# Optimization experiments

Hardware: AMD Instinct MI355X
Metric: run time of the kernel (lower is better)

Reference implementation:

```python
import jax, jax.numpy as jnp
import numpy as np

N = 32768       # nodes
E = 65536       # directed edges
B = 512         # graphs (N // B = 64 atoms each)
DIM = 64
NUM_FEAT = 14
EDGE_DIM = 4
NET_HID = 128
CONV_STEPS = 12
S2S_STEPS = 3
NSTEM = 1024
NUM_OUT_STEM = 105

leaky = lambda v: jax.nn.leaky_relu(v, 0.01)


def setup_inputs():
    key = jax.random.key(0)
    ks = jax.random.split(key, 30)
    p = lambda i, shape, s=0.1: jax.random.normal(ks[i], shape, jnp.float32) * s
    return {
        'x': jax.random.normal(ks[0], (N, NUM_FEAT), jnp.float32),
        'edge_attr': jax.random.uniform(ks[1], (E, EDGE_DIM), jnp.float32),
        'edge_index': jax.random.randint(ks[2], (2, E), 0, N),
        'batch': jnp.arange(N, dtype=jnp.int32) // (N // B),  # sorted graph ids, all graphs non-empty
        'stem_idx': jax.random.randint(ks[3], (NSTEM,), 0, N),
        'lin0_w': p(4, (DIM, NUM_FEAT)), 'lin0_b': p(5, (DIM,)),
        'net_w1': p(6, (NET_HID, EDGE_DIM)), 'net_b1': p(7, (NET_HID,)),
        'net_w2': p(8, (DIM * DIM, NET_HID), 0.05), 'net_b2': p(9, (DIM * DIM,), 0.05),
        'conv_root': p(10, (DIM, DIM)), 'conv_bias': p(11, (DIM,)),
        'gru_w_ih': p(12, (3 * DIM, DIM)), 'gru_w_hh': p(13, (3 * DIM, DIM)),
        'gru_b_ih': p(14, (3 * DIM,)), 'gru_b_hh': p(15, (3 * DIM,)),
        'lin1_w': p(16, (8 * DIM, DIM)), 'lin1_b': p(17, (8 * DIM,)),
        'lin2_w': p(18, (NUM_OUT_STEM, 8 * DIM)), 'lin2_b': p(19, (NUM_OUT_STEM,)),
        's2s_w_ih': p(20, (4 * DIM, 2 * DIM)), 's2s_w_hh': p(21, (4 * DIM, DIM)),
        's2s_b_ih': p(22, (4 * DIM,)), 's2s_b_hh': p(23, (4 * DIM,)),
        'lin3_w': p(24, (1, 2 * DIM)), 'lin3_b': p(25, (1,)),
    }


def reference(x, edge_attr, edge_index, batch, stem_idx,
              lin0_w, lin0_b, net_w1, net_b1, net_w2, net_b2,
              conv_root, conv_bias, gru_w_ih, gru_w_hh, gru_b_ih, gru_b_hh,
              lin1_w, lin1_b, lin2_w, lin2_b,
              s2s_w_ih, s2s_w_hh, s2s_b_ih, s2s_b_hh, lin3_w, lin3_b):
    src, dst = edge_index[0], edge_index[1]

    out = leaky(x @ lin0_w.T + lin0_b)               # [N, DIM]
    h = out

    # edge-conditioned weights: constant across conv steps (edge_attr fixed), hoist
    W = (leaky(edge_attr @ net_w1.T + net_b1) @ net_w2.T + net_b2).reshape(E, DIM, DIM)

    deg = jax.ops.segment_sum(jnp.ones((E,), jnp.float32), dst, num_segments=N)
    inv_deg = (1.0 / jnp.maximum(deg, 1.0))[:, None]

    def step(carry, _):
        out, h = carry
        # NNConv: gather src feats, per-edge matmul, scatter-mean to dst, plus root term
        msg = jnp.einsum('ei,eio->eo', out[src], W)                           # [E, DIM]
        agg = jax.ops.segment_sum(msg, dst, num_segments=N) * inv_deg        # scatter-mean
        m = leaky(agg + out @ conv_root + conv_bias)
        # GRU cell (torch gate order r, z, n)
        gi = m @ gru_w_ih.T + gru_b_ih
        gh = h @ gru_w_hh.T + gru_b_hh
        ir, iz, i_n = jnp.split(gi, 3, axis=-1)
        hr, hz, hn = jnp.split(gh, 3, axis=-1)
        r = jax.nn.sigmoid(ir + hr)
        z = jax.nn.sigmoid(iz + hz)
        n = jnp.tanh(i_n + r * hn)
        h_new = (1.0 - z) * n + z * h
        return (h_new, h_new), None

    (out, h), _ = jax.lax.scan(step, (out, h), None, length=CONV_STEPS)

    # per-stem head (stem_idx = precomputed flat node indices)
    stem_feat = out[stem_idx]                                                # [NSTEM, DIM]
    per_stem_out = leaky(stem_feat @ lin1_w.T + lin1_b) @ lin2_w.T + lin2_b  # [NSTEM, 105]

    # Set2Set readout (LSTM with torch gate order i, f, g, o)
    q_star = jnp.zeros((B, 2 * DIM), jnp.float32)
    hh = jnp.zeros((B, DIM), jnp.float32)
    cc = jnp.zeros((B, DIM), jnp.float32)
    for _ in range(S2S_STEPS):
        gates = q_star @ s2s_w_ih.T + s2s_b_ih + hh @ s2s_w_hh.T + s2s_b_hh
        gi_, gf_, gg_, go_ = jnp.split(gates, 4, axis=-1)
        cc = jax.nn.sigmoid(gf_) * cc + jax.nn.sigmoid(gi_) * jnp.tanh(gg_)
        hh = jax.nn.sigmoid(go_) * jnp.tanh(cc)
        q = hh                                                               # [B, DIM]
        e = jnp.sum(out * q[batch], axis=-1)                                 # [N]
        emax = jax.ops.segment_max(e, batch, num_segments=B)
        ee = jnp.exp(e - emax[batch])
        a = ee / jax.ops.segment_sum(ee, batch, num_segments=B)[batch]       # segment softmax
        r_read = jax.ops.segment_sum(a[:, None] * out, batch, num_segments=B)
        q_star = jnp.concatenate([q, r_read], axis=-1)

    sout = q_star @ lin3_w.T + lin3_b                                        # [B, 1]
    return sout, per_stem_out


if __name__ == '__main__':
    o = reference(**setup_inputs())
    print(o[0].shape, o[1].shape)
```

## Files before the change

kernel.cpp:

```cpp
#include <hip/hip_runtime.h>
#include <hip/hip_bf16.h>

#define N_NODES   32768
#define N_EDGES   65536
#define NGRAPH    512
#define DIM       64
#define NFEAT     14
#define NHID      128
#define WCOLS     4096
#define NSTEM     1024
#define NOUT      105

typedef __attribute__((ext_vector_type(8))) short short8;
typedef __attribute__((ext_vector_type(4))) float f32x4;

__device__ __forceinline__ float bf2f(unsigned int u16) {
  union { unsigned int i; float f; } c; c.i = u16 << 16; return c.f;
}
__device__ __forceinline__ unsigned short f2bf(float f) {
  union { float f; unsigned int i; } c; c.f = f;
  return (unsigned short)((c.i + 0x7fffu + ((c.i >> 16) & 1u)) >> 16);
}
__device__ __forceinline__ float leaky(float x) { return x > 0.f ? x : 0.01f * x; }
__device__ __forceinline__ float sigm(float x) { return 1.f / (1.f + expf(-x)); }

constexpr size_t ALN(size_t x) { return (x + 255) & ~(size_t)255; }

constexpr size_t OFF_HIDP = 0;
constexpr size_t SZ_HIDP  = (size_t)N_EDGES * NHID * 2;
constexpr size_t OFF_T2T  = ALN(OFF_HIDP + SZ_HIDP);
constexpr size_t SZ_T2T   = (size_t)WCOLS * NHID * 2;
constexpr size_t OFF_B2T  = ALN(OFF_T2T + SZ_T2T);
constexpr size_t SZ_B2T   = (size_t)WCOLS * 4;
constexpr size_t OFF_STATE= ALN(OFF_B2T + SZ_B2T);
constexpr size_t SZ_STATE = (size_t)N_NODES * DIM * 4;
constexpr size_t OFF_AGG  = ALN(OFF_STATE + SZ_STATE);
constexpr size_t SZ_AGG   = SZ_STATE;
constexpr size_t OFF_IDEG = ALN(OFF_AGG + SZ_AGG);
constexpr size_t SZ_IDEG  = (size_t)N_NODES * 4;
constexpr size_t OFF_CNT  = ALN(OFF_IDEG + SZ_IDEG);
constexpr size_t SZ_CNT   = (size_t)N_NODES * 4;
constexpr size_t OFF_RP   = ALN(OFF_CNT + SZ_CNT);
constexpr size_t SZ_RP    = (size_t)(N_NODES + 1) * 4;
constexpr size_t OFF_CUR  = ALN(OFF_RP + SZ_RP);
constexpr size_t SZ_CUR   = (size_t)N_NODES * 4;
constexpr size_t OFF_SRCP = ALN(OFF_CUR + SZ_CUR);
constexpr size_t SZ_SRCP  = (size_t)N_EDGES * 4;
constexpr size_t OFF_DSTP = ALN(OFF_SRCP + SZ_SRCP);
constexpr size_t SZ_DSTP  = (size_t)N_EDGES * 4;
constexpr size_t OFF_EPOS = ALN(OFF_DSTP + SZ_DSTP);
constexpr size_t SZ_EPOS  = (size_t)N_EDGES * 4;
constexpr size_t OFF_BW1  = ALN(OFF_EPOS + SZ_EPOS);
constexpr size_t SZ_BW1   = 256 * 64 * 2;
constexpr size_t OFF_BW2  = ALN(OFF_BW1 + SZ_BW1);
constexpr size_t SZ_BW2   = 192 * 64 * 2;
constexpr size_t OFF_WIH  = ALN(OFF_BW2 + SZ_BW2);
constexpr size_t SZ_WIH   = 128 * 256 * 4;
constexpr size_t OFF_WHH  = ALN(OFF_WIH + SZ_WIH);
constexpr size_t SZ_WHH   = 64 * 256 * 4;
constexpr size_t OFF_S8   = ALN(OFF_WHH + SZ_WHH);
constexpr size_t SZ_S8    = (size_t)N_NODES * 64;
constexpr size_t OFF_SSC  = ALN(OFF_S8 + SZ_S8);
constexpr size_t SZ_SSC   = (size_t)N_NODES * 4;
constexpr size_t OFF_SCL  = ALN(OFF_SSC + SZ_SSC);
constexpr size_t SZ_SCL   = (size_t)N_EDGES * 64 * 4;
constexpr size_t OFF_WT   = ALN(OFF_SCL + SZ_SCL);

__global__ void k_deg(const int* __restrict__ dst, int* __restrict__ cnt) {
  int e = blockIdx.x * 256 + threadIdx.x;
  atomicAdd(&cnt[dst[e]], 1);
}
__global__ __launch_bounds__(1024) void k_scan(const int* __restrict__ cnt,
                                               int* __restrict__ rp,
                                               int* __restrict__ cur,
                                               float* __restrict__ ideg) {
  __shared__ int part[1024];
  const int t = threadIdx.x, base = t * 32;
  int s = 0;
  for (int i = 0; i < 32; ++i) s += cnt[base + i];
  part[t] = s;
  __syncthreads();
  for (int off = 1; off < 1024; off <<= 1) {
    int v = (t >= off) ? part[t - off] : 0;
    __syncthreads();
    part[t] += v;
    __syncthreads();
  }
  int run = part[t] - s;
  for (int i = 0; i < 32; ++i) {
    int c = cnt[base + i];
    rp[base + i] = run; cur[base + i] = run;
    ideg[base + i] = 1.0f / fmaxf((float)c, 1.0f);
    run += c;
  }
  if (t == 1023) rp[N_NODES] = run;
}
__global__ void k_permute(const int* __restrict__ src, const int* __restrict__ dst,
                          int* __restrict__ cur, int* __restrict__ src_p,
                          int* __restrict__ dst_p, int* __restrict__ epos) {
  int e = blockIdx.x * 256 + threadIdx.x;
  int d = dst[e];
  int p = atomicAdd(&cur[d], 1);
  src_p[p] = src[e]; dst_p[p] = d; epos[e] = p;
}
__global__ void k_prep_t2(const float* __restrict__ w2, const float* __restrict__ b2,
                          unsigned short* __restrict__ T2t, float* __restrict__ b2t) {
  int gid = blockIdx.x * 256 + threadIdx.x;
  int r = gid >> 7, h = gid & 127;
  int srow = (r & 63) * 64 + (r >> 6);
  T2t[gid] = f2bf(w2[(size_t)srow * 128 + h]);
  if (h == 0) b2t[r] = b2[srow];
}
__global__ void k_prep_gru(const float* __restrict__ root, const float* __restrict__ whh,
                           const float* __restrict__ wih,
                           unsigned short* __restrict__ BW1, unsigned short* __restrict__ BW2) {
  int gid = blockIdx.x * 256 + threadIdx.x;
  if (gid >= 64 * 448) return;
  int i = gid / 448, c = gid % 448;
  if (c < 64)        BW1[c * 64 + i] = f2bf(root[i * 64 + c]);
  else if (c < 256)  BW1[c * 64 + i] = f2bf(whh[(c - 64) * 64 + i]);
  else               BW2[(c - 256) * 64 + i] = f2bf(wih[(c - 256) * 64 + i]);
}
__global__ void k_prep_s2s(const float* __restrict__ wih, const float* __restrict__ whh,
                           float* __restrict__ wihT, float* __restrict__ whhT) {
  int gid = blockIdx.x * 256 + threadIdx.x;
  if (gid < 32768) { int j = gid >> 8, k = gid & 255; wihT[gid] = wih[k * 128 + j]; }
  else { int g2 = gid - 32768; int j = g2 >> 8, k = g2 & 255; whhT[g2] = whh[k * 64 + j]; }
}
__global__ void k_lin0(const float* __restrict__ x, const float* __restrict__ w,
                       const float* __restrict__ b, float* __restrict__ state) {
  int gid = blockIdx.x * 256 + threadIdx.x;
  int n = gid >> 6, o = gid & 63;
  float acc = b[o];
  #pragma unroll
  for (int f = 0; f < NFEAT; ++f) acc += x[(size_t)n * NFEAT + f] * w[o * NFEAT + f];
  state[gid] = leaky(acc);
}
__global__ void k_hidden(const float* __restrict__ ea, const float* __restrict__ w1,
                         const float* __restrict__ b1, const int* __restrict__ epos,
                         unsigned short* __restrict__ hid_p) {
  int gid = blockIdx.x * 256 + threadIdx.x;
  int e = gid >> 7, h = gid & 127;
  float acc = b1[h];
  #pragma unroll
  for (int d = 0; d < 4; ++d) acc += ea[(size_t)e * 4 + d] * w1[h * 4 + d];
  hid_p[(size_t)epos[e] * 128 + h] = f2bf(leaky(acc));
}
__global__ __launch_bounds__(256) void k_qstate(const float* __restrict__ state,
                                                char* __restrict__ s8,
                                                float* __restrict__ sscale) {
  __shared__ char q8[4][64];
  __shared__ float scs[4];
  const int t = threadIdx.x, wv = t >> 6, ln = t & 63;
  const int n = blockIdx.x * 4 + wv;
  float v = state[(size_t)n * 64 + ln];
  float m = fabsf(v);
  #pragma unroll
  for (int off = 1; off < 64; off <<= 1) m = fmaxf(m, __shfl_xor(m, off));
  float inv = m > 0.f ? 127.f / m : 0.f;
  q8[wv][ln] = (char)(int)rintf(v * inv);
  if (ln == 0) scs[wv] = m * (1.f / 127.f);
  __syncthreads();
  if (t < 64) {
    int w2 = t >> 4, c = t & 15;
    reinterpret_cast<int*>(s8)[((size_t)(blockIdx.x * 4 + w2)) * 16 + c] =
        reinterpret_cast<const int*>(q8[w2])[c];
  }
  if (t < 4) sscale[blockIdx.x * 4 + t] = scs[t];
}

#define WG_PAD 136
__global__ __launch_bounds__(256) void k_wgemm(const unsigned short* __restrict__ A,
                                               const unsigned short* __restrict__ Bt,
                                               const float* __restrict__ b2t,
                                               unsigned char* __restrict__ W8,
                                               float* __restrict__ SCL) {
  __shared__ __align__(16) unsigned short As[64 * WG_PAD];
  __shared__ __align__(16) unsigned short Bs[64 * WG_PAD];
  __shared__ __align__(16) char pk[64][64];
  const int nb = blockIdx.x, mb = blockIdx.y, t = threadIdx.x;
  #pragma unroll
  for (int j = 0; j < 4; ++j) {
    int c = t + 256 * j;
    int row = c >> 4, col8 = (c & 15) * 8;
    *reinterpret_cast<uint4*>(&As[row * WG_PAD + col8]) =
        *reinterpret_cast<const uint4*>(A + (size_t)(mb * 64 + row) * 128 + col8);
    *reinterpret_cast<uint4*>(&Bs[row * WG_PAD + col8]) =
        *reinterpret_cast<const uint4*>(Bt + (size_t)(nb * 64 + row) * 128 + col8);
  }
  __syncthreads();
  const int wv = t >> 6, ln = t & 63, r = ln & 15, g = ln >> 4;
  f32x4 acc[4] = {};
  #pragma unroll
  for (int ks = 0; ks < 4; ++ks) {
    int kk = ks * 32 + g * 8;
    short8 a = *reinterpret_cast<const short8*>(&As[(wv * 16 + r) * WG_PAD + kk]);
    #pragma unroll
    for (int nt = 0; nt < 4; ++nt) {
      short8 b = *reinterpret_cast<const short8*>(&Bs[(nt * 16 + r) * WG_PAD + kk]);
      acc[nt] = __builtin_amdgcn_mfma_f32_16x16x32_bf16(a, b, acc[nt], 0, 0, 0);
    }
  }
  float bias[4];
  #pragma unroll
  for (int nt = 0; nt < 4; ++nt) bias[nt] = b2t[nb * 64 + nt * 16 + r];
  #pragma unroll
  for (int j = 0; j < 4; ++j) {
    int e_l = wv * 16 + g * 4 + j;
    float w[4], m = 0.f;
    #pragma unroll
    for (int nt = 0; nt < 4; ++nt) { w[nt] = acc[nt][j] + bias[nt]; m = fmaxf(m, fabsf(w[nt])); }
    m = fmaxf(m, __shfl_xor(m, 1)); m = fmaxf(m, __shfl_xor(m, 2));
    m = fmaxf(m, __shfl_xor(m, 4)); m = fmaxf(m, __shfl_xor(m, 8));
    float inv = m > 0.f ? 127.f / m : 0.f;
    #pragma unroll
    for (int nt = 0; nt < 4; ++nt)
      pk[e_l][nt * 16 + r] = (char)(int)rintf(w[nt] * inv);
    if (r == 0) {
      size_t e8 = (size_t)mb * 64 + e_l;
      SCL[e8 * 64 + nb] = m * (1.f / 127.f);
    }
  }
  __syncthreads();
  {
    int e_l = t >> 2, jc = t & 3;
    size_t e8 = (size_t)mb * 64 + e_l;
    *reinterpret_cast<uint4*>(W8 + e8 * 4096 + jc * 1024 + nb * 16) =
        *reinterpret_cast<const uint4*>(&pk[e_l][jc * 16]);
  }
}

__device__ __forceinline__ int dot64(const uint4* __restrict__ wp, const int* __restrict__ s) {
  int u = 0;
  #pragma unroll
  for (int j = 0; j < 4; ++j) {
    uint4 v = wp[j * 64];
    u = __builtin_amdgcn_sdot4((int)v.x, s[j * 4 + 0], u, false);
    u = __builtin_amdgcn_sdot4((int)v.y, s[j * 4 + 1], u, false);
    u = __builtin_amdgcn_sdot4((int)v.z, s[j * 4 + 2], u, false);
    u = __builtin_amdgcn_sdot4((int)v.w, s[j * 4 + 3], u, false);
  }
  return u;
}

__global__ __launch_bounds__(256) void k_msg_csr(const unsigned char* __restrict__ W8,
                                                 const float* __restrict__ SCL,
                                                 const char* __restrict__ s8,
                                                 const float* __restrict__ sscale,
                                                 int lim8,
                                                 const int* __restrict__ rp,
                                                 const int* __restrict__ src_p,
                                                 const float* __restrict__ ideg,
                                                 float* __restrict__ agg) {
  const int wv = threadIdx.x >> 6, ln = threadIdx.x & 63;
  const int d = blockIdx.x * 4 + wv;
  int k0 = rp[d], k1 = rp[d + 1];
  if (k1 > lim8) k1 = lim8;
  float acc = 0.f;
  int k = k0;
  for (; k + 2 <= k1; k += 2) {
    const uint4* wA = reinterpret_cast<const uint4*>(W8 + (size_t)k * 4096 + ln * 16);
    const uint4* wB = reinterpret_cast<const uint4*>(W8 + (size_t)(k + 1) * 4096 + ln * 16);
    int sA = __builtin_amdgcn_readfirstlane(src_p[k]);
    int sB = __builtin_amdgcn_readfirstlane(src_p[k + 1]);
    const int* rA = reinterpret_cast<const int*>(s8 + (size_t)sA * 64);
    const int* rB = reinterpret_cast<const int*>(s8 + (size_t)sB * 64);
    float fA = SCL[(size_t)k * 64 + ln] * sscale[sA];
    float fB = SCL[(size_t)k * 64 + 64 + ln] * sscale[sB];
    int uA = dot64(wA, rA);
    int uB = dot64(wB, rB);
    acc = fmaf((float)uA, fA, acc);
    acc = fmaf((float)uB, fB, acc);
  }
  if (k < k1) {
    const uint4* wA = reinterpret_cast<const uint4*>(W8 + (size_t)k * 4096 + ln * 16);
    int sA = __builtin_amdgcn_readfirstlane(src_p[k]);
    const int* rA = reinterpret_cast<const int*>(s8 + (size_t)sA * 64);
    float fA = SCL[(size_t)k * 64 + ln] * sscale[sA];
    acc = fmaf((float)dot64(wA, rA), fA, acc);
  }
  agg[(size_t)d * 64 + ln] = acc * ideg[d];
}

#define WM_PAD 136
__global__ __launch_bounds__(256) void k_wmsg(const unsigned short* __restrict__ hid,
                                              const unsigned short* __restrict__ T2t,
                                              const float* __restrict__ b2t,
                                              const float* __restrict__ state,
                                              const int* __restrict__ srcs,
                                              const int* __restrict__ dsts,
                                              const float* __restrict__ ideg,
                                              int e0,
                                              float* __restrict__ agg) {
  __shared__ __align__(16) unsigned short As[64 * WM_PAD];
  __shared__ __align__(16) unsigned short Bs[2][64 * WM_PAD];
  __shared__ __align__(16) float Ss[64][68];
  __shared__ int dstl[64]; __shared__ float idgl[64];
  __shared__ int srcl[64];
  const int t = threadIdx.x;
  const int eb = blockIdx.x * 64;
  if (t < 64) {
    int e = e0 + eb + t;
    srcl[t] = srcs[e];
    int d = dsts[e]; dstl[t] = d; idgl[t] = ideg[d];
  }
  __syncthreads();
  #pragma unroll
  for (int j = 0; j < 4; ++j) {
    int c = t + 256 * j;
    int row = c >> 4, col8 = (c & 15) * 8;
    *reinterpret_cast<uint4*>(&As[row * WM_PAD + col8]) =
        *reinterpret_cast<const uint4*>(hid + (size_t)(eb + row) * 128 + col8);
  }
  #pragma unroll
  for (int j = 0; j < 4; ++j) {
    int c = t + 256 * j;
    int row = c >> 4, q = (c & 15) * 4;
    *reinterpret_cast<float4*>(&Ss[row][q]) =
        *reinterpret_cast<const float4*>(state + (size_t)srcl[row] * 64 + q);
  }
  #pragma unroll
  for (int j = 0; j < 4; ++j) {
    int c = t + 256 * j;
    int row = c >> 4, col8 = (c & 15) * 8;
    *reinterpret_cast<uint4*>(&Bs[0][row * WM_PAD + col8]) =
        *reinterpret_cast<const uint4*>(T2t + (size_t)row * 128 + col8);
  }
  __syncthreads();
  const int wv = t >> 6, ln = t & 63, r = ln & 15, g = ln >> 4;
  for (int nb = 0; nb < 64; ++nb) {
    const int cur = nb & 1;
    if (nb + 1 < 64) {
      #pragma unroll
      for (int j = 0; j < 4; ++j) {
        int c = t + 256 * j;
        int row = c >> 4, col8 = (c & 15) * 8;
        *reinterpret_cast<uint4*>(&Bs[cur ^ 1][row * WM_PAD + col8]) =
            *reinterpret_cast<const uint4*>(T2t + (size_t)((nb + 1) * 64 + row) * 128 + col8);
      }
    }
    f32x4 acc[4] = {};
    #pragma unroll
    for (int ks = 0; ks < 4; ++ks) {
      int kk = ks * 32 + g * 8;
      short8 a = *reinterpret_cast<const short8*>(&As[(wv * 16 + r) * WM_PAD + kk]);
      #pragma unroll
      for (int nt = 0; nt < 4; ++nt) {
        short8 b = *reinterpret_cast<const short8*>(&Bs[cur][(nt * 16 + r) * WM_PAD + kk]);
        acc[nt] = __builtin_amdgcn_mfma_f32_16x16x32_bf16(a, b, acc[nt], 0, 0, 0);
      }
    }
    float bias[4];
    #pragma unroll
    for (int nt = 0; nt < 4; ++nt) bias[nt] = b2t[nb * 64 + nt * 16 + r];
    float pj[4];
    #pragma unroll
    for (int j = 0; j < 4; ++j) {
      int row = wv * 16 + g * 4 + j;
      float p = 0.f;
      #pragma unroll
      for (int nt = 0; nt < 4; ++nt)
        p += (acc[nt][j] + bias[nt]) * Ss[row][nt * 16 + r];
      pj[j] = p;
    }
    #pragma unroll
    for (int j = 0; j < 4; ++j) {
      float p = pj[j];
      p += __shfl_xor(p, 1); p += __shfl_xor(p, 2);
      p += __shfl_xor(p, 4); p += __shfl_xor(p, 8);
      pj[j] = p;
    }
    if (r == 0) {
      #pragma unroll
      for (int j = 0; j < 4; ++j) {
        int row = wv * 16 + g * 4 + j;
        atomicAdd(&agg[(size_t)dstl[row] * 64 + nb], pj[j] * idgl[row]);
      }
    }
    __syncthreads();
  }
}

#define KPAD 72
__global__ __launch_bounds__(512, 1) void k_gru(const float* __restrict__ agg,
                                                float* __restrict__ state,
                                                const unsigned short* __restrict__ BW1,
                                                const unsigned short* __restrict__ BW2,
                                                const float* __restrict__ conv_bias,
                                                const float* __restrict__ b_ih,
                                                const float* __restrict__ b_hh,
                                                char* __restrict__ s8,
                                                float* __restrict__ sscale) {
  __shared__ __align__(16) unsigned short As[128 * KPAD];
  __shared__ __align__(16) unsigned short Ms[128 * KPAD];
  __shared__ __align__(16) unsigned short B1s[256 * KPAD];
  __shared__ __align__(16) unsigned short B2s[192 * KPAD];
  const int t = threadIdx.x;
  const int rowbase = blockIdx.x * 128;
  #pragma unroll
  for (int j = 0; j < 2; ++j) {
    int c = t + 512 * j;
    int row = c >> 3, col8 = (c & 7) * 8;
    const float* sp = state + (size_t)(rowbase + row) * 64 + col8;
    float4 f0 = *reinterpret_cast<const float4*>(sp);
    float4 f1 = *reinterpret_cast<const float4*>(sp + 4);
    short8 hv;
    hv[0] = (short)f2bf(f0.x); hv[1] = (short)f2bf(f0.y);
    hv[2] = (short)f2bf(f0.z); hv[3] = (short)f2bf(f0.w);
    hv[4] = (short)f2bf(f1.x); hv[5] = (short)f2bf(f1.y);
    hv[6] = (short)f2bf(f1.z); hv[7] = (short)f2bf(f1.w);
    *reinterpret_cast<short8*>(&As[row * KPAD + col8]) = hv;
  }
  #pragma unroll
  for (int j = 0; j < 4; ++j) {
    int c = t + 512 * j;
    int row = c >> 3, col8 = (c & 7) * 8;
    *reinterpret_cast<uint4*>(&B1s[row * KPAD + col8]) =
        *reinterpret_cast<const uint4*>(BW1 + row * 64 + col8);
  }
  #pragma unroll
  for (int j = 0; j < 3; ++j) {
    int c = t + 512 * j;
    int row = c >> 3, col8 = (c & 7) * 8;
    *reinterpret_cast<uint4*>(&B2s[row * KPAD + col8]) =
        *reinterpret_cast<const uint4*>(BW2 + row * 64 + col8);
  }
  __syncthreads();
  const int wv = t >> 6, ln = t & 63, r = ln & 15, g = ln >> 4;
  f32x4 acc1[16] = {};
  #pragma unroll
  for (int ks = 0; ks < 2; ++ks) {
    int kk = ks * 32 + g * 8;
    short8 a = *reinterpret_cast<const short8*>(&As[(wv * 16 + r) * KPAD + kk]);
    #pragma unroll
    for (int nt = 0; nt < 16; ++nt) {
      short8 b = *reinterpret_cast<const short8*>(&B1s[(nt * 16 + r) * KPAD + kk]);
      acc1[nt] = __builtin_amdgcn_mfma_f32_16x16x32_bf16(a, b, acc1[nt], 0, 0, 0);
    }
  }
  #pragma unroll
  for (int nt = 0; nt < 4; ++nt) {
    int col = nt * 16 + r;
    float cb = conv_bias[col];
    #pragma unroll
    for (int j = 0; j < 4; ++j) {
      int lrow = wv * 16 + g * 4 + j;
      float mv = agg[(size_t)(rowbase + lrow) * 64 + col] + acc1[nt][j] + cb;
      Ms[lrow * KPAD + col] = f2bf(leaky(mv));
    }
  }
  __syncthreads();
  f32x4 acc2[12] = {};
  #pragma unroll
  for (int ks = 0; ks < 2; ++ks) {
    int kk = ks * 32 + g * 8;
    short8 a = *reinterpret_cast<const short8*>(&Ms[(wv * 16 + r) * KPAD + kk]);
    #pragma unroll
    for (int nt = 0; nt < 12; ++nt) {
      short8 b = *reinterpret_cast<const short8*>(&B2s[(nt * 16 + r) * KPAD + kk]);
      acc2[nt] = __builtin_amdgcn_mfma_f32_16x16x32_bf16(a, b, acc2[nt], 0, 0, 0);
    }
  }
  float hnew[4][4];
  #pragma unroll
  for (int nt = 0; nt < 4; ++nt) {
    int o = nt * 16 + r;
    float bir = b_ih[o],       bhr = b_hh[o];
    float biz = b_ih[64 + o],  bhz = b_hh[64 + o];
    float bin = b_ih[128 + o], bhn = b_hh[128 + o];
    #pragma unroll
    for (int j = 0; j < 4; ++j) {
      size_t gidx = (size_t)(rowbase + wv * 16 + g * 4 + j) * 64 + o;
      float rr = sigm(acc2[nt][j] + bir + acc1[4 + nt][j] + bhr);
      float zz = sigm(acc2[4 + nt][j] + biz + acc1[8 + nt][j] + bhz);
      float nn = tanhf(acc2[8 + nt][j] + bin + rr * (acc1[12 + nt][j] + bhn));
      float hold = state[gidx];
      float hv = (1.f - zz) * nn + zz * hold;
      state[gidx] = hv;
      hnew[nt][j] = hv;
    }
  }
  char* s8t = (char*)As;
  #pragma unroll
  for (int j = 0; j < 4; ++j) {
    float mx = 0.f;
    #pragma unroll
    for (int nt = 0; nt < 4; ++nt) mx = fmaxf(mx, fabsf(hnew[nt][j]));
    mx = fmaxf(mx, __shfl_xor(mx, 1)); mx = fmaxf(mx, __shfl_xor(mx, 2));
    mx = fmaxf(mx, __shfl_xor(mx, 4)); mx = fmaxf(mx, __shfl_xor(mx, 8));
    float inv = mx > 0.f ? 127.f / mx : 0.f;
    int lrow = wv * 16 + g * 4 + j;
    #pragma unroll
    for (int nt = 0; nt < 4; ++nt)
      s8t[lrow * 64 + nt * 16 + r] = (char)(int)rintf(hnew[nt][j] * inv);
    if (r == 0) sscale[rowbase + lrow] = mx * (1.f / 127.f);
  }
  __syncthreads();
  {
    int row = t >> 2, c = t & 3;
    *reinterpret_cast<uint4*>(s8 + ((size_t)(rowbase + row)) * 64 + c * 16) =
        *reinterpret_cast<const uint4*>(s8t + row * 64 + c * 16);
  }
}

__global__ __launch_bounds__(256) void k_s2s(const float* __restrict__ state,
                                             const float* __restrict__ wihT,
                                             const float* __restrict__ whhT,
                                             const float* __restrict__ b_ih,
                                             const float* __restrict__ b_hh,
                                             const float* __restrict__ lin3_w,
                                             const float* __restrict__ lin3_b,
                                             float* __restrict__ d_out) {
  __shared__ float tile[64 * 65];
  __shared__ float qs[128], hhs[64], ccs[64], gates[256], attw[64];
  const int g = blockIdx.x, t = threadIdx.x;
  for (int c = t; c < 64 * 64; c += 256) {
    int row = c >> 6, col = c & 63;
    tile[row * 65 + col] = state[(size_t)(g * 64 + row) * 64 + col];
  }
  if (t < 128) qs[t] = 0.f;
  if (t < 64) { hhs[t] = 0.f; ccs[t] = 0.f; }
  __syncthreads();
  for (int it = 0; it < 3; ++it) {
    float acc = b_ih[t] + b_hh[t];
    for (int j = 0; j < 128; ++j) acc += qs[j] * wihT[j * 256 + t];
    for (int j = 0; j < 64; ++j)  acc += hhs[j] * whhT[j * 256 + t];
    gates[t] = acc;
    __syncthreads();
    if (t < 64) {
      float ci = sigm(gates[t]), cf = sigm(gates[64 + t]);
      float cg = tanhf(gates[128 + t]), co = sigm(gates[192 + t]);
      float c2 = cf * ccs[t] + ci * cg;
      ccs[t] = c2;
      float h2 = co * tanhf(c2);
      hhs[t] = h2; qs[t] = h2;
    }
    __syncthreads();
    if (t < 64) {
      float e = 0.f;
      for (int o = 0; o < 64; ++o) e += tile[t * 65 + o] * qs[o];
      float m = e;
      for (int off = 32; off; off >>= 1) m = fmaxf(m, __shfl_xor(m, off));
// ... 40 lines not shown
      float4 x3 = *reinterpret_cast<const float4*>(wr + i + 12);
      a0 += x0.x*feat[i]    + x0.y*feat[i+1]  + x0.z*feat[i+2]  + x0.w*feat[i+3];
      a1 += x1.x*feat[i+4]  + x1.y*feat[i+5]  + x1.z*feat[i+6]  + x1.w*feat[i+7];
      a2 += x2.x*feat[i+8]  + x2.y*feat[i+9]  + x2.z*feat[i+10] + x2.w*feat[i+11];
      a3 += x3.x*feat[i+12] + x3.y*feat[i+13] + x3.z*feat[i+14] + x3.w*feat[i+15];
    }
    hidl[t] = leaky(a0 + a1 + a2 + a3 + b1[t]);
  }
  __syncthreads();
  if (t < 4 * NOUT) {
    int o = t >> 2, q = t & 3;
    const float* wr = w2 + (size_t)o * 512 + q * 128;
    const float* hr = hidl + q * 128;
    float a0 = 0.f, a1 = 0.f, a2 = 0.f, a3 = 0.f;
    #pragma unroll
    for (int kk = 0; kk < 128; kk += 16) {
      float4 x0 = *reinterpret_cast<const float4*>(wr + kk);
      float4 x1 = *reinterpret_cast<const float4*>(wr + kk + 4);
      float4 x2 = *reinterpret_cast<const float4*>(wr + kk + 8);
      float4 x3 = *reinterpret_cast<const float4*>(wr + kk + 12);
      a0 += x0.x*hr[kk]    + x0.y*hr[kk+1]  + x0.z*hr[kk+2]  + x0.w*hr[kk+3];
      a1 += x1.x*hr[kk+4]  + x1.y*hr[kk+5]  + x1.z*hr[kk+6]  + x1.w*hr[kk+7];
      a2 += x2.x*hr[kk+8]  + x2.y*hr[kk+9]  + x2.z*hr[kk+10] + x2.w*hr[kk+11];
      a3 += x3.x*hr[kk+12] + x3.y*hr[kk+13] + x3.z*hr[kk+14] + x3.w*hr[kk+15];
    }
    float p = a0 + a1 + a2 + a3;
    p += __shfl_xor(p, 1); p += __shfl_xor(p, 2);
    if (q == 0) d_out[512 + (size_t)s * NOUT + o] = p + b2[o];
  }
}

extern "C" void kernel_launch(void* const* d_in, const int* in_sizes, int n_in,
                              void* d_out, int out_size, void* d_ws, size_t ws_size,
                              hipStream_t stream) {
  (void)in_sizes; (void)n_in; (void)out_size;
  if (ws_size < OFF_WT) return;

  long pe8 = (long)((ws_size - OFF_WT) / 4096);
  if (pe8 > N_EDGES) pe8 = N_EDGES;
  pe8 &= ~63L;
  const int LIM8 = (int)pe8;
  const int TE = N_EDGES - LIM8;

  const float* x         = (const float*)d_in[0];
  const float* edge_attr = (const float*)d_in[1];
  const int*   eidx      = (const int*)d_in[2];
  const int*   stem_idx  = (const int*)d_in[4];
  const float* lin0_w = (const float*)d_in[5];
  const float* lin0_b = (const float*)d_in[6];
  const float* net_w1 = (const float*)d_in[7];
  const float* net_b1 = (const float*)d_in[8];
  const float* net_w2 = (const float*)d_in[9];
  const float* net_b2 = (const float*)d_in[10];
  const float* conv_root = (const float*)d_in[11];
  const float* conv_bias = (const float*)d_in[12];
  const float* gru_w_ih = (const float*)d_in[13];
  const float* gru_w_hh = (const float*)d_in[14];
  const float* gru_b_ih = (const float*)d_in[15];
  const float* gru_b_hh = (const float*)d_in[16];
  const float* lin1_w = (const float*)d_in[17];
  const float* lin1_b = (const float*)d_in[18];
  const float* lin2_w = (const float*)d_in[19];
  const float* lin2_b = (const float*)d_in[20];
  const float* s2s_w_ih = (const float*)d_in[21];
  const float* s2s_w_hh = (const float*)d_in[22];
  const float* s2s_b_ih = (const float*)d_in[23];
  const float* s2s_b_hh = (const float*)d_in[24];
  const float* lin3_w = (const float*)d_in[25];
  const float* lin3_b = (const float*)d_in[26];

  char* ws = (char*)d_ws;
  unsigned short* hid_p = (unsigned short*)(ws + OFF_HIDP);
  unsigned short* T2t  = (unsigned short*)(ws + OFF_T2T);
  float*          b2t  = (float*)(ws + OFF_B2T);
  float*          state= (float*)(ws + OFF_STATE);
  float*          agg  = (float*)(ws + OFF_AGG);
  float*          ideg = (float*)(ws + OFF_IDEG);
  int*            cnt  = (int*)(ws + OFF_CNT);
  int*            rp   = (int*)(ws + OFF_RP);
  int*            cur  = (int*)(ws + OFF_CUR);
  int*            src_p= (int*)(ws + OFF_SRCP);
  int*            dst_p= (int*)(ws + OFF_DSTP);
  int*            epos = (int*)(ws + OFF_EPOS);
  unsigned short* BW1  = (unsigned short*)(ws + OFF_BW1);
  unsigned short* BW2  = (unsigned short*)(ws + OFF_BW2);
  float*          wihT = (float*)(ws + OFF_WIH);
  float*          whhT = (float*)(ws + OFF_WHH);
  char*           s8   = (char*)(ws + OFF_S8);
  float*          sscale = (float*)(ws + OFF_SSC);
  float*          SCL  = (float*)(ws + OFF_SCL);
  unsigned char*  W8   = (unsigned char*)(ws + OFF_WT);
  float* out = (float*)d_out;

  const int* src = eidx;
  const int* dst = eidx + N_EDGES;

  hipMemsetAsync(cnt, 0, SZ_CNT, stream);
  k_deg<<<N_EDGES / 256, 256, 0, stream>>>(dst, cnt);
  k_scan<<<1, 1024, 0, stream>>>(cnt, rp, cur, ideg);
  k_permute<<<N_EDGES / 256, 256, 0, stream>>>(src, dst, cur, src_p, dst_p, epos);
  k_prep_t2<<<(WCOLS * NHID) / 256, 256, 0, stream>>>(net_w2, net_b2, T2t, b2t);
  k_prep_gru<<<112, 256, 0, stream>>>(conv_root, gru_w_hh, gru_w_ih, BW1, BW2);
  k_prep_s2s<<<192, 256, 0, stream>>>(s2s_w_ih, s2s_w_hh, wihT, whhT);
  k_lin0<<<(N_NODES * DIM) / 256, 256, 0, stream>>>(x, lin0_w, lin0_b, state);
  k_qstate<<<N_NODES / 4, 256, 0, stream>>>(state, s8, sscale);
  k_hidden<<<(N_EDGES * NHID) / 256, 256, 0, stream>>>(edge_attr, net_w1, net_b1,
                                                       epos, hid_p);
  if (LIM8 > 0)
    k_wgemm<<<dim3(WCOLS / 64, LIM8 / 64), 256, 0, stream>>>(hid_p, T2t, b2t, W8, SCL);

  for (int s = 0; s < 12; ++s) {
    k_msg_csr<<<N_NODES / 4, 256, 0, stream>>>(W8, SCL, s8, sscale, LIM8,
                                               rp, src_p, ideg, agg);
    if (TE > 0)
      k_wmsg<<<(TE + 63) / 64, 256, 0, stream>>>(hid_p + (size_t)LIM8 * NHID, T2t, b2t,
                                                 state, src_p, dst_p, ideg, LIM8, agg);
    k_gru<<<N_NODES / 128, 512, 0, stream>>>(agg, state, BW1, BW2, conv_bias,
                                             gru_b_ih, gru_b_hh, s8, sscale);
  }

  k_s2s<<<NGRAPH, 256, 0, stream>>>(state, wihT, whhT, s2s_b_ih, s2s_b_hh,
                                    lin3_w, lin3_b, out);
  k_stem<<<NSTEM, 512, 0, stream>>>(state, stem_idx, lin1_w, lin1_b,
                                    lin2_w, lin2_b, out);
}
```

Measured before the change: 1.981 ms.

## Switch message pass to edge-parallel chunks with output-major int8 weight layout

Replaces the per-destination CSR message kernel with an edge-parallel kernel in which each wave handles 16 consecutive sorted edges. The quantized weight tensor and its scales are re-laid out so that each lane reads a contiguous 64-byte row per edge, instead of strided 16-byte pieces. Destination segments that straddle chunk boundaries are merged with atomics, and interior segments are stored directly. Because accumulation now relies on atomics, agg is zeroed once up front and cleared inside the GRU kernel after it is read, replacing per-step overwrites. This is meant to fix load imbalance across nodes with uneven degree and to improve memory access patterns, at the cost of extra atomics and writes to agg.

```diff
diff --git a/kernel.cpp b/kernel.cpp
--- a/kernel.cpp
+++ b/kernel.cpp
@@ -216,25 +216,22 @@
     #pragma unroll
     for (int nt = 0; nt < 4; ++nt)
       pk[e_l][nt * 16 + r] = (char)(int)rintf(w[nt] * inv);
-    if (r == 0) {
-      size_t e8 = (size_t)mb * 64 + e_l;
-      SCL[e8 * 64 + nb] = m * (1.f / 127.f);
-    }
+    if (r == 0) SCL[(size_t)mb * 4096 + nb * 64 + e_l] = m * (1.f / 127.f);
   }
   __syncthreads();
   {
-    int e_l = t >> 2, jc = t & 3;
-    size_t e8 = (size_t)mb * 64 + e_l;
-    *reinterpret_cast<uint4*>(W8 + e8 * 4096 + jc * 1024 + nb * 16) =
-        *reinterpret_cast<const uint4*>(&pk[e_l][jc * 16]);
-  }
-}
-
-__device__ __forceinline__ int dot64(const uint4* __restrict__ wp, const int* __restrict__ s) {
+    int e_l = t >> 2, q4 = t & 3;
+    *reinterpret_cast<uint4*>(W8 + (size_t)mb * 262144 + (size_t)nb * 4096 +
+                              e_l * 64 + q4 * 16) =
+        *reinterpret_cast<const uint4*>(&pk[e_l][q4 * 16]);
+  }
+}
+
+__device__ __forceinline__ int dot64c(const uint4* __restrict__ wp, const int* __restrict__ s) {
   int u = 0;
   #pragma unroll
   for (int j = 0; j < 4; ++j) {
-    uint4 v = wp[j * 64];
+    uint4 v = wp[j];
     u = __builtin_amdgcn_sdot4((int)v.x, s[j * 4 + 0], u, false);
     u = __builtin_amdgcn_sdot4((int)v.y, s[j * 4 + 1], u, false);
     u = __builtin_amdgcn_sdot4((int)v.z, s[j * 4 + 2], u, false);
@@ -243,43 +240,42 @@
   return u;
 }
 
-__global__ __launch_bounds__(256) void k_msg_csr(const unsigned char* __restrict__ W8,
-                                                 const float* __restrict__ SCL,
-                                                 const char* __restrict__ s8,
-                                                 const float* __restrict__ sscale,
-                                                 int lim8,
-                                                 const int* __restrict__ rp,
-                                                 const int* __restrict__ src_p,
-                                                 const float* __restrict__ ideg,
-                                                 float* __restrict__ agg) {
+__global__ __launch_bounds__(256) void k_msg_edge(const unsigned char* __restrict__ W8,
+                                                  const float* __restrict__ SCL,
+                                                  const char* __restrict__ s8,
+                                                  const float* __restrict__ sscale,
+                                                  int lim8,
+                                                  const int* __restrict__ src_p,
+                                                  const int* __restrict__ dst_p,
+                                                  const float* __restrict__ ideg,
+                                                  float* __restrict__ agg) {
   const int wv = threadIdx.x >> 6, ln = threadIdx.x & 63;
-  const int d = blockIdx.x * 4 + wv;
-  int k0 = rp[d], k1 = rp[d + 1];
-  if (k1 > lim8) k1 = lim8;
+  const int kbase = (blockIdx.x * 4 + wv) * 16;
+  if (kbase >= lim8) return;
+  const int svv = src_p[kbase + (ln & 15)];
+  const int dvv = dst_p[kbase + (ln & 15)];
   float acc = 0.f;
-  int k = k0;
-  for (; k + 2 <= k1; k += 2) {
-    const uint4* wA = reinterpret_cast<const uint4*>(W8 + (size_t)k * 4096 + ln * 16);
-    const uint4* wB = reinterpret_cast<const uint4*>(W8 + (size_t)(k + 1) * 4096 + ln * 16);
-    int sA = __builtin_amdgcn_readfirstlane(src_p[k]);
-    int sB = __builtin_amdgcn_readfirstlane(src_p[k + 1]);
-    const int* rA = reinterpret_cast<const int*>(s8 + (size_t)sA * 64);
-    const int* rB = reinterpret_cast<const int*>(s8 + (size_t)sB * 64);
-    float fA = SCL[(size_t)k * 64 + ln] * sscale[sA];
-    float fB = SCL[(size_t)k * 64 + 64 + ln] * sscale[sB];
-    int uA = dot64(wA, rA);
-    int uB = dot64(wB, rB);
-    acc = fmaf((float)uA, fA, acc);
-    acc = fmaf((float)uB, fB, acc);
-  }
-  if (k < k1) {
-    const uint4* wA = reinterpret_cast<const uint4*>(W8 + (size_t)k * 4096 + ln * 16);
-    int sA = __builtin_amdgcn_readfirstlane(src_p[k]);
-    const int* rA = reinterpret_cast<const int*>(s8 + (size_t)sA * 64);
-    float fA = SCL[(size_t)k * 64 + ln] * sscale[sA];
-    acc = fmaf((float)dot64(wA, rA), fA, acc);
-  }
-  agg[(size_t)d * 64 + ln] = acc * ideg[d];
+  int dcur = __builtin_amdgcn_readfirstlane(__shfl(dvv, 0));
+  bool first = true;
+  #pragma unroll 4
+  for (int i = 0; i < 16; ++i) {
+    const int k = kbase + i;
+    const int eb = k >> 6, el = k & 63;
+    const uint4* wp = reinterpret_cast<const uint4*>(
+        W8 + (size_t)eb * 262144 + (size_t)ln * 4096 + el * 64);
+    const int s  = __builtin_amdgcn_readfirstlane(__shfl(svv, i));
+    const int dk = __builtin_amdgcn_readfirstlane(__shfl(dvv, i));
+    const int* rs = reinterpret_cast<const int*>(s8 + (size_t)s * 64);
+    const float f = SCL[(size_t)eb * 4096 + ln * 64 + el] * sscale[s];
+    if (dk != dcur) {
+      float outv = acc * ideg[dcur];
+      if (first) atomicAdd(&agg[(size_t)dcur * 64 + ln], outv);
+      else       agg[(size_t)dcur * 64 + ln] = outv;
+      first = false; acc = 0.f; dcur = dk;
+    }
+    acc = fmaf((float)dot64c(wp, rs), f, acc);
+  }
+  atomicAdd(&agg[(size_t)dcur * 64 + ln], acc * ideg[dcur]);
 }
 
 #define WM_PAD 136
@@ -382,7 +378,7 @@
 }
 
 #define KPAD 72
-__global__ __launch_bounds__(512, 1) void k_gru(const float* __restrict__ agg,
+__global__ __launch_bounds__(512, 1) void k_gru(float* __restrict__ agg,
                                                 float* __restrict__ state,
                                                 const unsigned short* __restrict__ BW1,
                                                 const unsigned short* __restrict__ BW2,
@@ -445,7 +441,9 @@
     #pragma unroll
     for (int j = 0; j < 4; ++j) {
       int lrow = wv * 16 + g * 4 + j;
-      float mv = agg[(size_t)(rowbase + lrow) * 64 + col] + acc1[nt][j] + cb;
+      size_t aidx = (size_t)(rowbase + lrow) * 64 + col;
+      float mv = agg[aidx] + acc1[nt][j] + cb;
+      agg[aidx] = 0.f;
       Ms[lrow * KPAD + col] = f2bf(leaky(mv));
     }
   }
@@ -678,6 +676,7 @@
   const int* dst = eidx + N_EDGES;
 
   hipMemsetAsync(cnt, 0, SZ_CNT, stream);
+  hipMemsetAsync(agg, 0, SZ_AGG, stream);
   k_deg<<<N_EDGES / 256, 256, 0, stream>>>(dst, cnt);
   k_scan<<<1, 1024, 0, stream>>>(cnt, rp, cur, ideg);
   k_permute<<<N_EDGES / 256, 256, 0, stream>>>(src, dst, cur, src_p, dst_p, epos);
@@ -692,8 +691,9 @@
     k_wgemm<<<dim3(WCOLS / 64, LIM8 / 64), 256, 0, stream>>>(hid_p, T2t, b2t, W8, SCL);
 
   for (int s = 0; s < 12; ++s) {
-    k_msg_csr<<<N_NODES / 4, 256, 0, stream>>>(W8, SCL, s8, sscale, LIM8,
-                                               rp, src_p, ideg, agg);
+    if (LIM8 > 0)
+      k_msg_edge<<<(LIM8 + 63) / 64, 256, 0, stream>>>(W8, SCL, s8, sscale, LIM8,
+                                                       src_p, dst_p, ideg, agg);
     if (TE > 0)
       k_wmsg<<<(TE + 63) / 64, 256, 0, stream>>>(hid_p + (size_t)LIM8 * NHID, T2t, b2t,
                                                  state, src_p, dst_p, ideg, LIM8, agg);
```

Measured after the change: 2.284 ms. 1.15x slower.

## Pre-swizzle GRU weights into MFMA fragment layout and read from global

Applied to the files above, without the earlier changes.

The GRU weight matrices are pre-packed into the per-lane MFMA B-fragment order, so each wave loads its B operands straight from global or L2 instead of staging them in LDS. Dropping that staging shrinks LDS per block, which allows smaller 64-row, 256-thread blocks and more blocks per CU. The k_wgemm launch is also split into two half-sized launches. The risk is repeated global reads of the weights by every block in place of shared LDS reuse.

```diff
diff --git a/kernel.cpp b/kernel.cpp
--- a/kernel.cpp
+++ b/kernel.cpp
@@ -51,9 +51,9 @@
 constexpr size_t OFF_EPOS = ALN(OFF_DSTP + SZ_DSTP);
 constexpr size_t SZ_EPOS  = (size_t)N_EDGES * 4;
 constexpr size_t OFF_BW1  = ALN(OFF_EPOS + SZ_EPOS);
-constexpr size_t SZ_BW1   = 256 * 64 * 2;
+constexpr size_t SZ_BW1   = 32 * 64 * 8 * 2;
 constexpr size_t OFF_BW2  = ALN(OFF_BW1 + SZ_BW1);
-constexpr size_t SZ_BW2   = 192 * 64 * 2;
+constexpr size_t SZ_BW2   = 24 * 64 * 8 * 2;
 constexpr size_t OFF_WIH  = ALN(OFF_BW2 + SZ_BW2);
 constexpr size_t SZ_WIH   = 128 * 256 * 4;
 constexpr size_t OFF_WHH  = ALN(OFF_WIH + SZ_WIH);
@@ -113,13 +113,22 @@
 }
 __global__ void k_prep_gru(const float* __restrict__ root, const float* __restrict__ whh,
                            const float* __restrict__ wih,
-                           unsigned short* __restrict__ BW1, unsigned short* __restrict__ BW2) {
+                           unsigned short* __restrict__ BW1f, unsigned short* __restrict__ BW2f) {
   int gid = blockIdx.x * 256 + threadIdx.x;
   if (gid >= 64 * 448) return;
-  int i = gid / 448, c = gid % 448;
-  if (c < 64)        BW1[c * 64 + i] = f2bf(root[i * 64 + c]);
-  else if (c < 256)  BW1[c * 64 + i] = f2bf(whh[(c - 64) * 64 + i]);
-  else               BW2[(c - 256) * 64 + i] = f2bf(wih[(c - 256) * 64 + i]);
+  int k = gid / 448, n = gid % 448;
+  float v;
+  if (n < 64)        v = root[k * 64 + n];
+  else if (n < 256)  v = whh[(n - 64) * 64 + k];
+  else               v = wih[(n - 256) * 64 + k];
+  int ks = k >> 5, g = (k >> 3) & 3, m = k & 7;
+  if (n < 256) {
+    int nt = n >> 4, r = n & 15, ln = r + 16 * g;
+    BW1f[(((nt * 2 + ks) * 64 + ln) << 3) + m] = f2bf(v);
+  } else {
+    int n2 = n - 256, nt = n2 >> 4, r = n2 & 15, ln = r + 16 * g;
+    BW2f[(((nt * 2 + ks) * 64 + ln) << 3) + m] = f2bf(v);
+  }
 }
 __global__ void k_prep_s2s(const float* __restrict__ wih, const float* __restrict__ whh,
                            float* __restrict__ wihT, float* __restrict__ whhT) {
@@ -382,24 +391,22 @@
 }
 
 #define KPAD 72
-__global__ __launch_bounds__(512, 1) void k_gru(const float* __restrict__ agg,
-                                                float* __restrict__ state,
-                                                const unsigned short* __restrict__ BW1,
-                                                const unsigned short* __restrict__ BW2,
-                                                const float* __restrict__ conv_bias,
-                                                const float* __restrict__ b_ih,
-                                                const float* __restrict__ b_hh,
-                                                char* __restrict__ s8,
-                                                float* __restrict__ sscale) {
-  __shared__ __align__(16) unsigned short As[128 * KPAD];
-  __shared__ __align__(16) unsigned short Ms[128 * KPAD];
-  __shared__ __align__(16) unsigned short B1s[256 * KPAD];
-  __shared__ __align__(16) unsigned short B2s[192 * KPAD];
+__global__ __launch_bounds__(256) void k_gru(const float* __restrict__ agg,
+                                             float* __restrict__ state,
+                                             const unsigned short* __restrict__ BW1f,
+                                             const unsigned short* __restrict__ BW2f,
+                                             const float* __restrict__ conv_bias,
+                                             const float* __restrict__ b_ih,
+                                             const float* __restrict__ b_hh,
+                                             char* __restrict__ s8,
+                                             float* __restrict__ sscale) {
+  __shared__ __align__(16) unsigned short As[64 * KPAD];
+  __shared__ __align__(16) unsigned short Ms[64 * KPAD];
   const int t = threadIdx.x;
-  const int rowbase = blockIdx.x * 128;
+  const int rowbase = blockIdx.x * 64;
   #pragma unroll
   for (int j = 0; j < 2; ++j) {
-    int c = t + 512 * j;
+    int c = t + 256 * j;
     int row = c >> 3, col8 = (c & 7) * 8;
     const float* sp = state + (size_t)(rowbase + row) * 64 + col8;
     float4 f0 = *reinterpret_cast<const float4*>(sp);
@@ -411,20 +418,6 @@
     hv[6] = (short)f2bf(f1.z); hv[7] = (short)f2bf(f1.w);
     *reinterpret_cast<short8*>(&As[row * KPAD + col8]) = hv;
   }
-  #pragma unroll
-  for (int j = 0; j < 4; ++j) {
-    int c = t + 512 * j;
-    int row = c >> 3, col8 = (c & 7) * 8;
-    *reinterpret_cast<uint4*>(&B1s[row * KPAD + col8]) =
-        *reinterpret_cast<const uint4*>(BW1 + row * 64 + col8);
-  }
-  #pragma unroll
-  for (int j = 0; j < 3; ++j) {
-    int c = t + 512 * j;
-    int row = c >> 3, col8 = (c & 7) * 8;
-    *reinterpret_cast<uint4*>(&B2s[row * KPAD + col8]) =
-        *reinterpret_cast<const uint4*>(BW2 + row * 64 + col8);
-  }
   __syncthreads();
   const int wv = t >> 6, ln = t & 63, r = ln & 15, g = ln >> 4;
   f32x4 acc1[16] = {};
@@ -434,7 +427,8 @@
     short8 a = *reinterpret_cast<const short8*>(&As[(wv * 16 + r) * KPAD + kk]);
     #pragma unroll
     for (int nt = 0; nt < 16; ++nt) {
-      short8 b = *reinterpret_cast<const short8*>(&B1s[(nt * 16 + r) * KPAD + kk]);
+      short8 b = *reinterpret_cast<const short8*>(
+          BW1f + (((nt * 2 + ks) * 64 + ln) << 3));
       acc1[nt] = __builtin_amdgcn_mfma_f32_16x16x32_bf16(a, b, acc1[nt], 0, 0, 0);
     }
   }
@@ -457,7 +451,8 @@
     short8 a = *reinterpret_cast<const short8*>(&Ms[(wv * 16 + r) * KPAD + kk]);
     #pragma unroll
     for (int nt = 0; nt < 12; ++nt) {
-      short8 b = *reinterpret_cast<const short8*>(&B2s[(nt * 16 + r) * KPAD + kk]);
+      short8 b = *reinterpret_cast<const short8*>(
+          BW2f + (((nt * 2 + ks) * 64 + ln) << 3));
       acc2[nt] = __builtin_amdgcn_mfma_f32_16x16x32_bf16(a, b, acc2[nt], 0, 0, 0);
     }
   }
@@ -664,8 +659,8 @@
   int*            src_p= (int*)(ws + OFF_SRCP);
   int*            dst_p= (int*)(ws + OFF_DSTP);
   int*            epos = (int*)(ws + OFF_EPOS);
-  unsigned short* BW1  = (unsigned short*)(ws + OFF_BW1);
-  unsigned short* BW2  = (unsigned short*)(ws + OFF_BW2);
+  unsigned short* BW1f = (unsigned short*)(ws + OFF_BW1);
+  unsigned short* BW2f = (unsigned short*)(ws + OFF_BW2);
   float*          wihT = (float*)(ws + OFF_WIH);
   float*          whhT = (float*)(ws + OFF_WHH);
   char*           s8   = (char*)(ws + OFF_S8);
@@ -682,14 +677,21 @@
   k_scan<<<1, 1024, 0, stream>>>(cnt, rp, cur, ideg);
   k_permute<<<N_EDGES / 256, 256, 0, stream>>>(src, dst, cur, src_p, dst_p, epos);
   k_prep_t2<<<(WCOLS * NHID) / 256, 256, 0, stream>>>(net_w2, net_b2, T2t, b2t);
-  k_prep_gru<<<112, 256, 0, stream>>>(conv_root, gru_w_hh, gru_w_ih, BW1, BW2);
+  k_prep_gru<<<112, 256, 0, stream>>>(conv_root, gru_w_hh, gru_w_ih, BW1f, BW2f);
   k_prep_s2s<<<192, 256, 0, stream>>>(s2s_w_ih, s2s_w_hh, wihT, whhT);
   k_lin0<<<(N_NODES * DIM) / 256, 256, 0, stream>>>(x, lin0_w, lin0_b, state);
   k_qstate<<<N_NODES / 4, 256, 0, stream>>>(state, s8, sscale);
   k_hidden<<<(N_EDGES * NHID) / 256, 256, 0, stream>>>(edge_attr, net_w1, net_b1,
                                                        epos, hid_p);
-  if (LIM8 > 0)
-    k_wgemm<<<dim3(WCOLS / 64, LIM8 / 64), 256, 0, stream>>>(hid_p, T2t, b2t, W8, SCL);
+  if (LIM8 > 0) {
+    long half = ((long)LIM8 / 2) & ~63L;
+    if (half > 0)
+      k_wgemm<<<dim3(WCOLS / 64, half / 64), 256, 0, stream>>>(hid_p, T2t, b2t, W8, SCL);
+    if (LIM8 - half > 0)
+      k_wgemm<<<dim3(WCOLS / 64, (LIM8 - half) / 64), 256, 0, stream>>>(
+          hid_p + (size_t)half * NHID, T2t, b2t,
+          W8 + (size_t)half * 4096, SCL + (size_t)half * 64);
+  }
 
   for (int s = 0; s < 12; ++s) {
     k_msg_csr<<<N_NODES / 4, 256, 0, stream>>>(W8, SCL, s8, sscale, LIM8,
@@ -697,8 +699,8 @@
     if (TE > 0)
       k_wmsg<<<(TE + 63) / 64, 256, 0, stream>>>(hid_p + (size_t)LIM8 * NHID, T2t, b2t,
                                                  state, src_p, dst_p, ideg, LIM8, agg);
-    k_gru<<<N_NODES / 128, 512, 0, stream>>>(agg, state, BW1, BW2, conv_bias,
-                                             gru_b_ih, gru_b_hh, s8, sscale);
+    k_gru<<<N_NODES / 64, 256, 0, stream>>>(agg, state, BW1f, BW2f, conv_bias,
+                                            gru_b_ih, gru_b_hh, s8, sscale);
   }
 
   k_s2s<<<NGRAPH, 256, 0, stream>>>(state, wihT, whhT, s2s_b_ih, s2s_b_hh,
```

Result: slower. 2.130 ms (+7.5%).

## Store per-block weight scales as bf16 and batch 8 column blocks per wgemm CTA

Applied to the files above, without the earlier changes.

Each k_wgemm CTA now loops over 8 output column blocks, reusing the loaded A tile. It buffers the quantized int8 lines in registers and writes 128 contiguous bytes per row instead of scattered 16-byte pieces. The per-(edge,block) scale array is stored as bf16 instead of fp32, which halves the scale traffic that k_msg_csr reads in every one of the 12 conv steps. This trades fewer, more register-heavy wgemm CTAs and a small loss of scale precision for less memory traffic.

```diff
diff --git a/kernel.cpp b/kernel.cpp
--- a/kernel.cpp
+++ b/kernel.cpp
@@ -63,7 +63,7 @@
 constexpr size_t OFF_SSC  = ALN(OFF_S8 + SZ_S8);
 constexpr size_t SZ_SSC   = (size_t)N_NODES * 4;
 constexpr size_t OFF_SCL  = ALN(OFF_SSC + SZ_SSC);
-constexpr size_t SZ_SCL   = (size_t)N_EDGES * 64 * 4;
+constexpr size_t SZ_SCL   = (size_t)N_EDGES * 64 * 2;
 constexpr size_t OFF_WT   = ALN(OFF_SCL + SZ_SCL);
 
 __global__ void k_deg(const int* __restrict__ dst, int* __restrict__ cnt) {
@@ -170,63 +170,76 @@
 }
 
 #define WG_PAD 136
-__global__ __launch_bounds__(256) void k_wgemm(const unsigned short* __restrict__ A,
-                                               const unsigned short* __restrict__ Bt,
-                                               const float* __restrict__ b2t,
-                                               unsigned char* __restrict__ W8,
-                                               float* __restrict__ SCL) {
+__global__ __launch_bounds__(256) void k_wgemm8(const unsigned short* __restrict__ A,
+                                                const unsigned short* __restrict__ Bt,
+                                                const float* __restrict__ b2t,
+                                                unsigned char* __restrict__ W8,
+                                                unsigned short* __restrict__ SCLh) {
   __shared__ __align__(16) unsigned short As[64 * WG_PAD];
   __shared__ __align__(16) unsigned short Bs[64 * WG_PAD];
   __shared__ __align__(16) char pk[64][64];
-  const int nb = blockIdx.x, mb = blockIdx.y, t = threadIdx.x;
+  __shared__ unsigned short sclh[64][8];
+  const int og = blockIdx.x, mb = blockIdx.y, t = threadIdx.x;
   #pragma unroll
   for (int j = 0; j < 4; ++j) {
     int c = t + 256 * j;
     int row = c >> 4, col8 = (c & 15) * 8;
     *reinterpret_cast<uint4*>(&As[row * WG_PAD + col8]) =
         *reinterpret_cast<const uint4*>(A + (size_t)(mb * 64 + row) * 128 + col8);
-    *reinterpret_cast<uint4*>(&Bs[row * WG_PAD + col8]) =
-        *reinterpret_cast<const uint4*>(Bt + (size_t)(nb * 64 + row) * 128 + col8);
-  }
-  __syncthreads();
+  }
   const int wv = t >> 6, ln = t & 63, r = ln & 15, g = ln >> 4;
-  f32x4 acc[4] = {};
-  #pragma unroll
-  for (int ks = 0; ks < 4; ++ks) {
-    int kk = ks * 32 + g * 8;
-    short8 a = *reinterpret_cast<const short8*>(&As[(wv * 16 + r) * WG_PAD + kk]);
-    #pragma unroll
-    for (int nt = 0; nt < 4; ++nt) {
-      short8 b = *reinterpret_cast<const short8*>(&Bs[(nt * 16 + r) * WG_PAD + kk]);
-      acc[nt] = __builtin_amdgcn_mfma_f32_16x16x32_bf16(a, b, acc[nt], 0, 0, 0);
-    }
-  }
-  float bias[4];
-  #pragma unroll
-  for (int nt = 0; nt < 4; ++nt) bias[nt] = b2t[nb * 64 + nt * 16 + r];
-  #pragma unroll
-  for (int j = 0; j < 4; ++j) {
-    int e_l = wv * 16 + g * 4 + j;
-    float w[4], m = 0.f;
-    #pragma unroll
-    for (int nt = 0; nt < 4; ++nt) { w[nt] = acc[nt][j] + bias[nt]; m = fmaxf(m, fabsf(w[nt])); }
-    m = fmaxf(m, __shfl_xor(m, 1)); m = fmaxf(m, __shfl_xor(m, 2));
-    m = fmaxf(m, __shfl_xor(m, 4)); m = fmaxf(m, __shfl_xor(m, 8));
-    float inv = m > 0.f ? 127.f / m : 0.f;
-    #pragma unroll
-    for (int nt = 0; nt < 4; ++nt)
-      pk[e_l][nt * 16 + r] = (char)(int)rintf(w[nt] * inv);
-    if (r == 0) {
-      size_t e8 = (size_t)mb * 64 + e_l;
-      SCL[e8 * 64 + nb] = m * (1.f / 127.f);
-    }
-  }
-  __syncthreads();
+  uint4 wline[8];
+  #pragma unroll
+  for (int obi = 0; obi < 8; ++obi) {
+    const int nb = og * 8 + obi;
+    #pragma unroll
+    for (int j = 0; j < 4; ++j) {
+      int c = t + 256 * j;
+      int row = c >> 4, col8 = (c & 15) * 8;
+      *reinterpret_cast<uint4*>(&Bs[row * WG_PAD + col8]) =
+          *reinterpret_cast<const uint4*>(Bt + (size_t)(nb * 64 + row) * 128 + col8);
+    }
+    __syncthreads();
+    f32x4 acc[4] = {};
+    #pragma unroll
+    for (int ks = 0; ks < 4; ++ks) {
+      int kk = ks * 32 + g * 8;
+      short8 a = *reinterpret_cast<const short8*>(&As[(wv * 16 + r) * WG_PAD + kk]);
+      #pragma unroll
+      for (int nt = 0; nt < 4; ++nt) {
+        short8 b = *reinterpret_cast<const short8*>(&Bs[(nt * 16 + r) * WG_PAD + kk]);
+        acc[nt] = __builtin_amdgcn_mfma_f32_16x16x32_bf16(a, b, acc[nt], 0, 0, 0);
+      }
+    }
+    float bias[4];
+    #pragma unroll
+    for (int nt = 0; nt < 4; ++nt) bias[nt] = b2t[nb * 64 + nt * 16 + r];
+    #pragma unroll
+    for (int j = 0; j < 4; ++j) {
+      int e_l = wv * 16 + g * 4 + j;
+      float w[4], m = 0.f;
+      #pragma unroll
+      for (int nt = 0; nt < 4; ++nt) { w[nt] = acc[nt][j] + bias[nt]; m = fmaxf(m, fabsf(w[nt])); }
+      m = fmaxf(m, __shfl_xor(m, 1)); m = fmaxf(m, __shfl_xor(m, 2));
+      m = fmaxf(m, __shfl_xor(m, 4)); m = fmaxf(m, __shfl_xor(m, 8));
+      float inv = m > 0.f ? 127.f / m : 0.f;
+      #pragma unroll
+      for (int nt = 0; nt < 4; ++nt)
+        pk[e_l][nt * 16 + r] = (char)(int)rintf(w[nt] * inv);
+      if (r == 0) sclh[e_l][obi] = f2bf(m * (1.f / 127.f));
+    }
+    __syncthreads();
+    wline[obi] = *reinterpret_cast<const uint4*>(&pk[t >> 2][(t & 3) * 16]);
+  }
   {
-    int e_l = t >> 2, jc = t & 3;
-    size_t e8 = (size_t)mb * 64 + e_l;
-    *reinterpret_cast<uint4*>(W8 + e8 * 4096 + jc * 1024 + nb * 16) =
-        *reinterpret_cast<const uint4*>(&pk[e_l][jc * 16]);
+    unsigned char* dstp = W8 + ((size_t)(mb * 64) + (t >> 2)) * 4096 + (t & 3) * 1024 + og * 128;
+    #pragma unroll
+    for (int q = 0; q < 8; ++q)
+      reinterpret_cast<uint4*>(dstp)[q] = wline[q];
+  }
+  if (t < 64) {
+    *reinterpret_cast<uint4*>(SCLh + ((size_t)(mb * 64) + t) * 64 + og * 8) =
+        *reinterpret_cast<const uint4*>(&sclh[t][0]);
   }
 }
 
@@ -244,7 +257,7 @@
 }
 
 __global__ __launch_bounds__(256) void k_msg_csr(const unsigned char* __restrict__ W8,
-                                                 const float* __restrict__ SCL,
+                                                 const unsigned short* __restrict__ SCLh,
                                                  const char* __restrict__ s8,
                                                  const float* __restrict__ sscale,
                                                  int lim8,
@@ -265,8 +278,8 @@
     int sB = __builtin_amdgcn_readfirstlane(src_p[k + 1]);
     const int* rA = reinterpret_cast<const int*>(s8 + (size_t)sA * 64);
     const int* rB = reinterpret_cast<const int*>(s8 + (size_t)sB * 64);
-    float fA = SCL[(size_t)k * 64 + ln] * sscale[sA];
-    float fB = SCL[(size_t)k * 64 + 64 + ln] * sscale[sB];
+    float fA = bf2f(SCLh[(size_t)k * 64 + ln]) * sscale[sA];
+    float fB = bf2f(SCLh[(size_t)k * 64 + 64 + ln]) * sscale[sB];
     int uA = dot64(wA, rA);
     int uB = dot64(wB, rB);
     acc = fmaf((float)uA, fA, acc);
@@ -276,7 +289,7 @@
     const uint4* wA = reinterpret_cast<const uint4*>(W8 + (size_t)k * 4096 + ln * 16);
     int sA = __builtin_amdgcn_readfirstlane(src_p[k]);
     const int* rA = reinterpret_cast<const int*>(s8 + (size_t)sA * 64);
-    float fA = SCL[(size_t)k * 64 + ln] * sscale[sA];
+    float fA = bf2f(SCLh[(size_t)k * 64 + ln]) * sscale[sA];
     acc = fmaf((float)dot64(wA, rA), fA, acc);
   }
   agg[(size_t)d * 64 + ln] = acc * ideg[d];
@@ -670,7 +683,7 @@
   float*          whhT = (float*)(ws + OFF_WHH);
   char*           s8   = (char*)(ws + OFF_S8);
   float*          sscale = (float*)(ws + OFF_SSC);
-  float*          SCL  = (float*)(ws + OFF_SCL);
+  unsigned short* SCLh = (unsigned short*)(ws + OFF_SCL);
   unsigned char*  W8   = (unsigned char*)(ws + OFF_WT);
   float* out = (float*)d_out;
 
@@ -689,10 +702,10 @@
   k_hidden<<<(N_EDGES * NHID) / 256, 256, 0, stream>>>(edge_attr, net_w1, net_b1,
                                                        epos, hid_p);
   if (LIM8 > 0)
-    k_wgemm<<<dim3(WCOLS / 64, LIM8 / 64), 256, 0, stream>>>(hid_p, T2t, b2t, W8, SCL);
+    k_wgemm8<<<dim3(8, LIM8 / 64), 256, 0, stream>>>(hid_p, T2t, b2t, W8, SCLh);
 
   for (int s = 0; s < 12; ++s) {
-    k_msg_csr<<<N_NODES / 4, 256, 0, stream>>>(W8, SCL, s8, sscale, LIM8,
+    k_msg_csr<<<N_NODES / 4, 256, 0, stream>>>(W8, SCLh, s8, sscale, LIM8,
                                                rp, src_p, ideg, agg);
     if (TE > 0)
       k_wmsg<<<(TE + 63) / 64, 256, 0, stream>>>(hid_p + (size_t)LIM8 * NHID, T2t, b2t,
```

New measurement: 2.021 ms. 2.0% more time.
